# Kernel tuning notes

Measured on AMD Instinct MI355X. Metric: run time of the kernel, lower is better.

## Reference

```python
import jax, jax.numpy as jnp
import numpy as np


def setup_inputs() -> dict:
    key = jax.random.key(0)
    k1, k2, k3 = jax.random.split(key, 3)
    B, C, P = 16384, 2048, 256
    f_struct = jax.random.normal(k1, (B, C), dtype=jnp.float32)
    pids = jax.random.randint(k2, (B,), 0, P, dtype=jnp.int64)
    camids = jax.random.randint(k3, (B,), 0, 2, dtype=jnp.int64)
    return {"f_struct": f_struct, "pids": pids, "camids": camids, "num_pids": P}


def reference(f_struct, pids, camids, num_pids):
    # Fused segment reduction over joint (pid, camid) groups: seg = pid*2 + camid
    seg = (pids * 2 + camids).astype(jnp.int32)
    n_seg = num_pids * 2
    sums = jax.ops.segment_sum(f_struct, seg, num_segments=n_seg)          # [2P, C]
    counts = jax.ops.segment_sum(jnp.ones_like(seg, dtype=f_struct.dtype),
                                 seg, num_segments=n_seg)                   # [2P]
    means = sums / jnp.maximum(counts, 1)[:, None]                          # safe mean
    means = means.reshape(num_pids, 2, -1)                                  # [P, 2, C]
    counts = counts.reshape(num_pids, 2)                                    # [P, 2]
    # per-pid MSE between visible (cam 0) and thermal (cam 1) centers
    diff = means[:, 0, :] - means[:, 1, :]
    mse = jnp.mean(diff * diff, axis=-1)                                    # [P]
    valid = (counts[:, 0] > 0) & (counts[:, 1] > 0)                         # [P]
    cnt = jnp.sum(valid.astype(f_struct.dtype))
    loss = jnp.sum(jnp.where(valid, mse, 0.0)) / jnp.maximum(cnt, 1)
    return jnp.where(cnt > 0, loss, jnp.zeros((), dtype=f_struct.dtype))
```

## Files before the change

kernel.cpp:

```cpp
#include <hip/hip_runtime.h>

#define NPID   256
#define CCOLS  2048
#define NCHUNK 2
#define CHUNKW 1024
#define CAP    1024


__device__ __forceinline__ void gather_cam(const float* __restrict__ base,
                                           const int* __restrict__ list,
                                           int cnt, float4& acc)
{
    int n8 = cnt & ~7;
    if (n8 > 0) {
        float4 v[8];
#pragma unroll
        for (int k = 0; k < 8; ++k)
            v[k] = *reinterpret_cast<const float4*>(base + (size_t)list[k] * CCOLS);
        for (int i = 8; i < n8; i += 8) {
            float4 w[8];
#pragma unroll
            for (int k = 0; k < 8; ++k)
                w[k] = *reinterpret_cast<const float4*>(base + (size_t)list[i + k] * CCOLS);
#pragma unroll
            for (int k = 0; k < 8; ++k) {
                acc.x += v[k].x; acc.y += v[k].y; acc.z += v[k].z; acc.w += v[k].w;
                v[k] = w[k];
            }
        }
#pragma unroll
        for (int k = 0; k < 8; ++k) {
            acc.x += v[k].x; acc.y += v[k].y; acc.z += v[k].z; acc.w += v[k].w;
        }
    }
    for (int i = n8; i < cnt; ++i) {
        float4 vv = *reinterpret_cast<const float4*>(base + (size_t)list[i] * CCOLS);
        acc.x += vv.x; acc.y += vv.y; acc.z += vv.z; acc.w += vv.w;
    }
}

__global__ __launch_bounds__(256) void gather_k(
    const float* __restrict__ f, const int* __restrict__ pids,
    const int* __restrict__ camids, float* __restrict__ part,
    float* __restrict__ vflag, int B)
{
    __shared__ int list0[CAP], list1[CAP];
    __shared__ int cur0, cur1;

    int p     = blockIdx.x >> 1;
    int chunk = blockIdx.x & 1;
    int t     = threadIdx.x;

    if (t == 0) { cur0 = 0; cur1 = 0; }
    __syncthreads();

    for (int i = t; i < B; i += 256) {
        if (pids[i] == p) {
            if (camids[i] == 0) {
                int pos = atomicAdd(&cur0, 1);
                if (pos < CAP) list0[pos] = i;
            } else {
                int pos = atomicAdd(&cur1, 1);
                if (pos < CAP) list1[pos] = i;
            }
        }
    }
    __syncthreads();
    int c0 = min(cur0, CAP), c1 = min(cur1, CAP);

    const float* base = f + (size_t)chunk * CHUNKW + (size_t)t * 4;
    float4 acc0 = make_float4(0.f, 0.f, 0.f, 0.f);
    float4 acc1 = make_float4(0.f, 0.f, 0.f, 0.f);
    gather_cam(base, list0, c0, acc0);
    gather_cam(base, list1, c1, acc1);

    float i0 = 1.0f / (float)(c0 > 0 ? c0 : 1);
    float i1 = 1.0f / (float)(c1 > 0 ? c1 : 1);
    float dx = acc0.x * i0 - acc1.x * i1;
    float dy = acc0.y * i0 - acc1.y * i1;
    float dz = acc0.z * i0 - acc1.z * i1;
    float dw = acc0.w * i0 - acc1.w * i1;
    float sq = dx * dx + dy * dy + dz * dz + dw * dw;

    for (int off = 32; off; off >>= 1) sq += __shfl_down(sq, off);
    __shared__ float wred[4];
    if ((t & 63) == 0) wred[t >> 6] = sq;
    __syncthreads();
    if (t == 0) {
        part[blockIdx.x] = wred[0] + wred[1] + wred[2] + wred[3];
        if (chunk == 0) vflag[p] = (c0 > 0 && c1 > 0) ? 1.0f : 0.0f;
    }
}

__global__ __launch_bounds__(256) void reduce_k(
    const float* __restrict__ part, const float* __restrict__ vflag,
    float* __restrict__ out)
{
    int t = threadIdx.x;
    float mse   = (part[2 * t] + part[2 * t + 1]) * (1.0f / (float)CCOLS);
    float valid = vflag[t];
    float num   = valid * mse;
    float cv    = valid;
    for (int off = 32; off; off >>= 1) {
        num += __shfl_down(num, off);
        cv  += __shfl_down(cv, off);
    }
    __shared__ float nred[4], cred[4];
    if ((t & 63) == 0) { nred[t >> 6] = num; cred[t >> 6] = cv; }
    __syncthreads();
    if (t == 0) {
        float N  = nred[0] + nred[1] + nred[2] + nred[3];
        float Cv = cred[0] + cred[1] + cred[2] + cred[3];
        out[0] = (Cv > 0.0f) ? (N / fmaxf(Cv, 1.0f)) : 0.0f;
    }
}

extern "C" void kernel_launch(void* const* d_in, const int* in_sizes, int n_in,
                              void* d_out, int out_size, void* d_ws, size_t ws_size,
                              hipStream_t stream)
{
    const float* f      = (const float*)d_in[0];
    const int*   pids   = (const int*)d_in[1];
    const int*   camids = (const int*)d_in[2];

    int B = in_sizes[1];

    float* part  = (float*)d_ws;
    float* vflag = (float*)((char*)d_ws + 2048);

    gather_k<<<NPID * NCHUNK, 256, 0, stream>>>(f, pids, camids, part, vflag, B);
    reduce_k<<<1, 256, 0, stream>>>(part, vflag, (float*)d_out);
}
```

Measured before the change: 223.7 us.

## Use one 1024-thread block per pid with float2 gather and vectorized index scan

Replaces the two 256-thread blocks per pid (each owning half the columns) with a single 1024-thread block per pid, where each thread reads a float2 across the full row. Index building now loads pids/camids as int4, and the gather uses readfirstlane on row indices plus a software-pipelined prefetch of 8 rows separated by sched barriers. This halves the redundant full scan of pids/camids per block and aims for more memory-level parallelism in the row gather. In exchange it launches only 256 blocks, which may underfill the GPU, and lowers the list capacity to 512, which assumes no group exceeds that size.

```diff
diff --git a/kernel.cpp b/kernel.cpp
--- a/kernel.cpp
+++ b/kernel.cpp
@@ -1,106 +1,115 @@
 #include <hip/hip_runtime.h>
 
-#define NPID   256
-#define CCOLS  2048
-#define NCHUNK 2
-#define CHUNKW 1024
-#define CAP    1024
+#define NPID 256
+#define CC   2048
+#define CCH  (CC / 2)
+#define TPB  1024
+#define CAP  512
+#define PIPE 8
 
+__device__ __forceinline__ float2 seg_stream(const float2* __restrict__ f2,
+                                             const int* __restrict__ list,
+                                             int c, int t)
+{
+    float2 acc = make_float2(0.f, 0.f);
+    if (c <= 0) return acc;
 
-__device__ __forceinline__ void gather_cam(const float* __restrict__ base,
-                                           const int* __restrict__ list,
-                                           int cnt, float4& acc)
-{
-    int n8 = cnt & ~7;
-    if (n8 > 0) {
-        float4 v[8];
+    float2 buf[PIPE];
 #pragma unroll
-        for (int k = 0; k < 8; ++k)
-            v[k] = *reinterpret_cast<const float4*>(base + (size_t)list[k] * CCOLS);
-        for (int i = 8; i < n8; i += 8) {
-            float4 w[8];
+    for (int k = 0; k < PIPE; ++k) {
+        int idx = (k < c) ? k : (c - 1);
+        int r = __builtin_amdgcn_readfirstlane(list[idx]);
+        buf[k] = f2[(size_t)r * CCH + t];
+    }
+    __builtin_amdgcn_sched_barrier(0);
+
+    int i = 0;
+    for (; i + PIPE <= c; ) {
+        float2 cur[PIPE];
 #pragma unroll
-            for (int k = 0; k < 8; ++k)
-                w[k] = *reinterpret_cast<const float4*>(base + (size_t)list[i + k] * CCOLS);
+        for (int k = 0; k < PIPE; ++k) cur[k] = buf[k];
+        i += PIPE;
 #pragma unroll
-            for (int k = 0; k < 8; ++k) {
-                acc.x += v[k].x; acc.y += v[k].y; acc.z += v[k].z; acc.w += v[k].w;
-                v[k] = w[k];
-            }
+        for (int k = 0; k < PIPE; ++k) {
+            int idx = (i + k < c) ? (i + k) : (c - 1);
+            int r = __builtin_amdgcn_readfirstlane(list[idx]);
+            buf[k] = f2[(size_t)r * CCH + t];
         }
+        __builtin_amdgcn_sched_barrier(0);
 #pragma unroll
-        for (int k = 0; k < 8; ++k) {
-            acc.x += v[k].x; acc.y += v[k].y; acc.z += v[k].z; acc.w += v[k].w;
-        }
+        for (int k = 0; k < PIPE; ++k) { acc.x += cur[k].x; acc.y += cur[k].y; }
     }
-    for (int i = n8; i < cnt; ++i) {
-        float4 vv = *reinterpret_cast<const float4*>(base + (size_t)list[i] * CCOLS);
-        acc.x += vv.x; acc.y += vv.y; acc.z += vv.z; acc.w += vv.w;
+#pragma unroll
+    for (int k = 0; k < PIPE; ++k) {
+        if (i + k < c) { acc.x += buf[k].x; acc.y += buf[k].y; }
     }
+    return acc;
 }
 
-__global__ __launch_bounds__(256) void gather_k(
+__global__ __launch_bounds__(TPB) void main_k(
     const float* __restrict__ f, const int* __restrict__ pids,
-    const int* __restrict__ camids, float* __restrict__ part,
-    float* __restrict__ vflag, int B)
+    const int* __restrict__ camids, float* __restrict__ mse,
+    float* __restrict__ valid, int B)
 {
     __shared__ int list0[CAP], list1[CAP];
-    __shared__ int cur0, cur1;
+    __shared__ int cnt0_s, cnt1_s;
 
-    int p     = blockIdx.x >> 1;
-    int chunk = blockIdx.x & 1;
-    int t     = threadIdx.x;
+    const int p = blockIdx.x;
+    const int t = threadIdx.x;
 
-    if (t == 0) { cur0 = 0; cur1 = 0; }
+    if (t == 0) { cnt0_s = 0; cnt1_s = 0; }
     __syncthreads();
 
-    for (int i = t; i < B; i += 256) {
-        if (pids[i] == p) {
-            if (camids[i] == 0) {
-                int pos = atomicAdd(&cur0, 1);
-                if (pos < CAP) list0[pos] = i;
-            } else {
-                int pos = atomicAdd(&cur1, 1);
-                if (pos < CAP) list1[pos] = i;
-            }
-        }
+    const int4* p4 = reinterpret_cast<const int4*>(pids);
+    const int4* c4 = reinterpret_cast<const int4*>(camids);
+    const int nv = B >> 2;
+    for (int i = t; i < nv; i += TPB) {
+        int4 pv = p4[i];
+        int4 cv = c4[i];
+        int base = i << 2;
+        if (pv.x == p) { int pos = atomicAdd(cv.x ? &cnt1_s : &cnt0_s, 1);
+                         if (pos < CAP) (cv.x ? list1 : list0)[pos] = base; }
+        if (pv.y == p) { int pos = atomicAdd(cv.y ? &cnt1_s : &cnt0_s, 1);
+                         if (pos < CAP) (cv.y ? list1 : list0)[pos] = base + 1; }
+        if (pv.z == p) { int pos = atomicAdd(cv.z ? &cnt1_s : &cnt0_s, 1);
+                         if (pos < CAP) (cv.z ? list1 : list0)[pos] = base + 2; }
+        if (pv.w == p) { int pos = atomicAdd(cv.w ? &cnt1_s : &cnt0_s, 1);
+                         if (pos < CAP) (cv.w ? list1 : list0)[pos] = base + 3; }
     }
     __syncthreads();
-    int c0 = min(cur0, CAP), c1 = min(cur1, CAP);
+    const int c0 = min(cnt0_s, CAP), c1 = min(cnt1_s, CAP);
 
-    const float* base = f + (size_t)chunk * CHUNKW + (size_t)t * 4;
-    float4 acc0 = make_float4(0.f, 0.f, 0.f, 0.f);
-    float4 acc1 = make_float4(0.f, 0.f, 0.f, 0.f);
-    gather_cam(base, list0, c0, acc0);
-    gather_cam(base, list1, c1, acc1);
+    const float2* f2 = reinterpret_cast<const float2*>(f);
+    float2 a0 = seg_stream(f2, list0, c0, t);
+    float2 a1 = seg_stream(f2, list1, c1, t);
 
-    float i0 = 1.0f / (float)(c0 > 0 ? c0 : 1);
-    float i1 = 1.0f / (float)(c1 > 0 ? c1 : 1);
-    float dx = acc0.x * i0 - acc1.x * i1;
-    float dy = acc0.y * i0 - acc1.y * i1;
-    float dz = acc0.z * i0 - acc1.z * i1;
-    float dw = acc0.w * i0 - acc1.w * i1;
-    float sq = dx * dx + dy * dy + dz * dz + dw * dw;
+    const float i0 = 1.0f / (float)(c0 > 0 ? c0 : 1);
+    const float i1 = 1.0f / (float)(c1 > 0 ? c1 : 1);
+    const float dx = a0.x * i0 - a1.x * i1;
+    const float dy = a0.y * i0 - a1.y * i1;
+    float sq = dx * dx + dy * dy;
 
     for (int off = 32; off; off >>= 1) sq += __shfl_down(sq, off);
-    __shared__ float wred[4];
+    __shared__ float wred[TPB / 64];
     if ((t & 63) == 0) wred[t >> 6] = sq;
     __syncthreads();
     if (t == 0) {
-        part[blockIdx.x] = wred[0] + wred[1] + wred[2] + wred[3];
-        if (chunk == 0) vflag[p] = (c0 > 0 && c1 > 0) ? 1.0f : 0.0f;
+        float tot = 0.f;
+#pragma unroll
+        for (int w = 0; w < TPB / 64; ++w) tot += wred[w];
+        mse[p]   = tot;
+        valid[p] = (c0 > 0 && c1 > 0) ? 1.0f : 0.0f;
     }
 }
 
 __global__ __launch_bounds__(256) void reduce_k(
-    const float* __restrict__ part, const float* __restrict__ vflag,
+    const float* __restrict__ mse, const float* __restrict__ valid,
     float* __restrict__ out)
 {
     int t = threadIdx.x;
-    float mse   = (part[2 * t] + part[2 * t + 1]) * (1.0f / (float)CCOLS);
-    float valid = vflag[t];
-    float num   = valid * mse;
-    float cv    = valid;
+    float v   = valid[t];
+    float num = v * mse[t] * (1.0f / (float)CC);
+    float cv  = v;
     for (int off = 32; off; off >>= 1) {
         num += __shfl_down(num, off);
         cv  += __shfl_down(cv, off);
@@ -125,9 +134,9 @@
 
     int B = in_sizes[1];
 
-    float* part  = (float*)d_ws;
-    float* vflag = (float*)((char*)d_ws + 2048);
+    float* mse   = (float*)d_ws;
+    float* valid = (float*)((char*)d_ws + 1024);
 
-    gather_k<<<NPID * NCHUNK, 256, 0, stream>>>(f, pids, camids, part, vflag, B);
-    reduce_k<<<1, 256, 0, stream>>>(part, vflag, (float*)d_out);
+    main_k<<<NPID, TPB, 0, stream>>>(f, pids, camids, mse, valid, B);
+    reduce_k<<<1, 256, 0, stream>>>(mse, valid, (float*)d_out);
 }
```

Result: faster. 202.9 us (-9.3%).
